# Optimization experiments

Measured on AMD Instinct MI355X. Metric: run time of the kernel, lower is better.

Reference implementation:

```python
import jax, jax.numpy as jnp
import numpy as np

B, C, F, D, K = 128, 64, 129, 512, 8192  # batch, channels, stft bins, d_model, codebook size


def setup_inputs() -> dict:
    key = jax.random.key(0)
    k0, k1, k2, k3 = jax.random.split(key, 4)
    x = jax.random.normal(k0, (B, C, F), dtype=jnp.float32)
    # nn.Linear(129, 512): weight stored transposed here as [F, D] for einsum
    W = jax.random.normal(k1, (F, D), dtype=jnp.float32) * (1.0 / np.sqrt(F).astype(np.float32))
    b = jnp.zeros((D,), dtype=jnp.float32)
    codebook = jax.random.normal(k2, (K, D), dtype=jnp.float32)
    pos_emb = jax.random.normal(k3, (1, C, D), dtype=jnp.float32)
    return {"x": x, "W": W, "b": b, "codebook": codebook, "pos_emb": pos_emb}


def reference(x, W, b, codebook, pos_emb):
    # Linear projection: [B,C,F] @ [F,D] -> [B,C,D]
    z = jnp.einsum('bcf,fd->bcd', x, W) + b

    # Vector quantization: nearest codebook entry by squared L2 distance.
    # dist(z,e) = |z|^2 - 2 z.e + |e|^2; argmin unaffected by constant |z|^2 per token,
    # but keep full expression for faithfulness/numerics.
    z2 = jnp.sum(z * z, axis=-1, keepdims=True)              # [B,C,1]
    e2 = jnp.sum(codebook * codebook, axis=-1)               # [K]
    dots = jnp.einsum('bcd,kd->bck', z, codebook)            # [B,C,K] dominant GEMM
    dists = z2 - 2.0 * dots + e2                             # [B,C,K]
    idx = jnp.argmin(dists, axis=-1)                         # [B,C] int
    q = codebook[idx]                                        # gather: [B,C,D]

    # commitment loss: mse(stop_grad(quantize), z)
    commit_loss = jnp.mean(jnp.square(jax.lax.stop_gradient(q) - z))

    # straight-through estimator
    quantized = z + jax.lax.stop_gradient(q - z)

    out = quantized + pos_emb
    return out, commit_loss
```

## Files before the change

### kernel.cpp

```cpp
#include <hip/hip_runtime.h>
#include <hip/hip_bf16.h>
#include <hip/hip_fp16.h>
#include <stdint.h>

#define B_ 128
#define C_ 64
#define F_ 129
#define D_ 512
#define K_ 8192
#define M_ (B_ * C_)

typedef __attribute__((ext_vector_type(8))) _Float16 half8;
typedef __attribute__((ext_vector_type(4))) float f32x4;
typedef unsigned long long u64;

__device__ __forceinline__ ushort f2h(float f) {
  const _Float16 h = (_Float16)f;
  return __builtin_bit_cast(ushort, h);
}
__device__ __forceinline__ uint32_t fmap(float f) {
  uint32_t s = __float_as_uint(f);
  return s ^ ((s & 0x80000000u) ? 0xFFFFFFFFu : 0x80000000u);
}

__global__ __launch_bounds__(256) void k_prep(
    const float* __restrict__ x, const float* __restrict__ W,
    const float* __restrict__ bias, const float* __restrict__ cb,
    float* __restrict__ z, ushort* __restrict__ zf, ushort* __restrict__ cf,
    float* __restrict__ e2) {
  const int tid = threadIdx.x;
  if (blockIdx.x < 512) {
    __shared__ float xs[16][F_];
    const int t0 = blockIdx.x * 16;
    const float* xsrc = x + (size_t)t0 * F_;
    for (int i = tid; i < 16 * F_; i += 256) xs[i / F_][i % F_] = xsrc[i];
    __syncthreads();
    float a0[16], a1[16];
#pragma unroll
    for (int r = 0; r < 16; ++r) { a0[r] = 0.f; a1[r] = 0.f; }
    const int c0 = tid, c1 = tid + 256;
    for (int f = 0; f < F_; ++f) {
      const float w0 = W[f * D_ + c0];
      const float w1 = W[f * D_ + c1];
#pragma unroll
      for (int r = 0; r < 16; ++r) {
        const float xv = xs[r][f];
        a0[r] = __builtin_fmaf(xv, w0, a0[r]);
        a1[r] = __builtin_fmaf(xv, w1, a1[r]);
      }
    }
    const float b0 = bias[c0], b1 = bias[c1];
#pragma unroll
    for (int r = 0; r < 16; ++r) {
      const size_t row = (size_t)(t0 + r) * D_;
      const float v0 = a0[r] + b0, v1 = a1[r] + b1;
      z[row + c0] = v0;
      z[row + c1] = v1;
      zf[row + c0] = f2h(v0);
      zf[row + c1] = f2h(v1);
    }
  } else {
    const int row = (blockIdx.x - 512) * 4 + (tid >> 6);
    const int lane = tid & 63;
    const float* src = cb + (size_t)row * D_;
    float s = 0.f;
#pragma unroll
    for (int i = 0; i < 8; ++i) {
      const int d = lane + i * 64;
      const float v = src[d];
      s = __builtin_fmaf(v, v, s);
      cf[(size_t)row * D_ + d] = f2h(v);
    }
#pragma unroll
    for (int o = 32; o > 0; o >>= 1) s += __shfl_down(s, o);
    if (lane == 0) e2[row] = s;
  }
}

__device__ __forceinline__ void stage_tile(const ushort* __restrict__ g,
                                           int r0, int k0, ushort* lds,
                                           int tid) {
  const int c = tid & 7;
#pragma unroll
  for (int i = 0; i < 4; ++i) {
    const int r = i * 32 + (tid >> 3);
    const int cs = c ^ (r & 7);
    const ushort* src = g + (size_t)(r0 + r) * D_ + k0 + cs * 8;
    char* dst = (char*)lds + i * 4096 + (tid >> 6) * 1024;
    __builtin_amdgcn_global_load_lds(
        (const __attribute__((address_space(1))) void*)src,
        (__attribute__((address_space(3))) void*)dst, 16, 0, 0);
  }
}

__global__ __launch_bounds__(256, 4) void k_argmin(
    const ushort* __restrict__ zf, const ushort* __restrict__ cf,
    const float* __restrict__ e2, u64* __restrict__ blk2) {
  __shared__ ushort lA[128 * 64], lB[128 * 64];
  const int tid = threadIdx.x;
  const int lane = tid & 63;
  const int w = tid >> 6;
  const int wr = (w >> 1) * 64;
  const int wc = (w & 1) * 64;
  const int m0 = (blockIdx.x >> 6) * 128;
  const int n0 = (blockIdx.x & 63) * 128;

  f32x4 acc[4][4];
#pragma unroll
  for (int m = 0; m < 4; ++m)
#pragma unroll
    for (int n = 0; n < 4; ++n) acc[m][n] = (f32x4){0.f, 0.f, 0.f, 0.f};

  for (int kt = 0; kt < D_ / 64; ++kt) {
    __syncthreads();
    stage_tile(zf, m0, kt * 64, lA, tid);
    stage_tile(cf, n0, kt * 64, lB, tid);
    asm volatile("s_waitcnt vmcnt(0)" ::: "memory");
    __syncthreads();
#pragma unroll
    for (int ks = 0; ks < 2; ++ks) {
      half8 at[4], bc[4];
#pragma unroll
      for (int m = 0; m < 4; ++m) {
        const int row = wr + m * 16 + (lane & 15);
        const int cbo = (ks * 64 + ((lane >> 4) << 4)) ^ ((row & 7) << 4);
        at[m] = *(const half8*)((const char*)lA + row * 128 + cbo);
      }
#pragma unroll
      for (int n = 0; n < 4; ++n) {
        const int row = wc + n * 16 + (lane & 15);
        const int cbo = (ks * 64 + ((lane >> 4) << 4)) ^ ((row & 7) << 4);
        bc[n] = *(const half8*)((const char*)lB + row * 128 + cbo);
      }
#pragma unroll
      for (int mc = 0; mc < 4; ++mc)
#pragma unroll
        for (int nt = 0; nt < 4; ++nt)
          acc[mc][nt] = __builtin_amdgcn_mfma_f32_16x16x32_f16(
              bc[mc], at[nt], acc[mc][nt], 0, 0, 0);
    }
  }

  const int cbase = n0 + wc + ((lane >> 4) << 2);
  float e2r[4][4];
#pragma unroll
  for (int mc = 0; mc < 4; ++mc)
#pragma unroll
    for (int j = 0; j < 4; ++j) e2r[mc][j] = e2[cbase + mc * 16 + j];
  const int half = (n0 + wc) >> 6;
  const int tbase = m0 + wr;

#pragma unroll
  for (int nt = 0; nt < 4; ++nt) {
    float v1 = 3.0e38f, v2 = 3.0e38f;
    int i1 = 0, i2 = 0;
#pragma unroll
    for (int mc = 0; mc < 4; ++mc) {
#pragma unroll
      for (int j = 0; j < 4; ++j) {
        const float dd = __builtin_fmaf(-2.f, acc[mc][nt][j], e2r[mc][j]);
        const int ii = cbase + mc * 16 + j;
        const bool lt1 = dd < v1;
        const bool lt2 = dd < v2;
        v2 = lt1 ? v1 : (lt2 ? dd : v2);
        i2 = lt1 ? i1 : (lt2 ? ii : i2);
        v1 = lt1 ? dd : v1;
        i1 = lt1 ? ii : i1;
      }
    }
#pragma unroll
    for (int o = 16; o < 64; o <<= 1) {
      const float bv1 = __shfl_xor(v1, o), bv2 = __shfl_xor(v2, o);
      const int bi1 = __shfl_xor(i1, o), bi2 = __shfl_xor(i2, o);
      const bool t = bv1 < v1;
      const float hv = t ? v1 : bv1;
      const int hi = t ? i1 : bi1;
      v1 = t ? bv1 : v1;
      i1 = t ? bi1 : i1;
      const bool t2 = bv2 < v2;
      const float cv2 = t2 ? bv2 : v2;
      const int ci2 = t2 ? bi2 : i2;
      const bool t3 = hv < cv2;
      v2 = t3 ? hv : cv2;
      i2 = t3 ? hi : ci2;
    }
    if (lane < 16) {
      const int row = tbase + nt * 16 + lane;
      u64* dst = blk2 + (size_t)row * 256 + half * 2;
      dst[0] = ((u64)fmap(v1) << 32) | (uint32_t)i1;
      dst[1] = ((u64)fmap(v2) << 32) | (uint32_t)i2;
    }
  }
}

#define CS(a, b)                          \
  {                                       \
    const u64 lo_ = (a < b) ? a : b;      \
    const u64 hi_ = (a < b) ? b : a;      \
    a = lo_;                              \
    b = hi_;                              \
  }

__global__ __launch_bounds__(256) void k_resolve(
    const u64* __restrict__ blk2, const float* __restrict__ cb,
    const float* __restrict__ z, const float* __restrict__ pos,
    float* __restrict__ out, float* __restrict__ lossp) {
  const int t = blockIdx.x * 4 + (threadIdx.x >> 6);
  const int lane = threadIdx.x & 63;
  const u64* kp = blk2 + (size_t)t * 256;
  u64 v0 = kp[lane * 4 + 0], v1 = kp[lane * 4 + 1];
  u64 v2 = kp[lane * 4 + 2], v3 = kp[lane * 4 + 3];
  CS(v0, v1) CS(v2, v3) CS(v0, v2) CS(v1, v3) CS(v1, v2)
#pragma unroll
  for (int o = 1; o < 64; o <<= 1) {
    const u64 b0 = __shfl_xor(v0, o), b1 = __shfl_xor(v1, o);
    const u64 b2 = __shfl_xor(v2, o), b3 = __shfl_xor(v3, o);
    u64 m0 = (v0 < b3) ? v0 : b3;
    u64 m1 = (v1 < b2) ? v1 : b2;
    u64 m2 = (v2 < b1) ? v2 : b1;
    u64 m3 = (v3 < b0) ? v3 : b0;
    CS(m0, m2) CS(m1, m3) CS(m0, m1) CS(m2, m3)
    v0 = m0; v1 = m1; v2 = m2; v3 = m3;
  }
  const int i0 = (int)(v0 & 0xFFFFFFFFull);
  const int i1 = (int)(v1 & 0xFFFFFFFFull);
  const int i2 = (int)(v2 & 0xFFFFFFFFull);
  const int i3 = (int)(v3 & 0xFFFFFFFFull);
  const float* c0 = cb + (size_t)i0 * D_;
  const float* c1 = cb + (size_t)i1 * D_;
  const float* c2 = cb + (size_t)i2 * D_;
  const float* c3 = cb + (size_t)i3 * D_;
  const float* zr = z + (size_t)t * D_;
  float zv[8], c0v[8], c1v[8], c2v[8], c3v[8];
  double dt0 = 0.0, dt1 = 0.0, dt2 = 0.0, dt3 = 0.0;
  double q0 = 0.0, q1 = 0.0, q2 = 0.0, q3 = 0.0;
#pragma unroll
  for (int i = 0; i < 8; ++i) {
    const int d = lane + i * 64;
    zv[i] = zr[d];
    c0v[i] = c0[d]; c1v[i] = c1[d]; c2v[i] = c2[d]; c3v[i] = c3[d];
    dt0 += (double)zv[i] * (double)c0v[i]; q0 += (double)c0v[i] * (double)c0v[i];
    dt1 += (double)zv[i] * (double)c1v[i]; q1 += (double)c1v[i] * (double)c1v[i];
    dt2 += (double)zv[i] * (double)c2v[i]; q2 += (double)c2v[i] * (double)c2v[i];
    dt3 += (double)zv[i] * (double)c3v[i]; q3 += (double)c3v[i] * (double)c3v[i];
  }
#pragma unroll
  for (int o = 1; o < 64; o <<= 1) {
    dt0 += __shfl_xor(dt0, o); dt1 += __shfl_xor(dt1, o);
    dt2 += __shfl_xor(dt2, o); dt3 += __shfl_xor(dt3, o);
    q0 += __shfl_xor(q0, o); q1 += __shfl_xor(q1, o);
    q2 += __shfl_xor(q2, o); q3 += __shfl_xor(q3, o);
  }
  const double d0 = q0 - 2.0 * dt0;
  const double d1 = q1 - 2.0 * dt1;
  const double d2 = q2 - 2.0 * dt2;
  const double d3 = q3 - 2.0 * dt3;
  int bsel = 0, bidx = i0;
  double bd = d0;
  if (d1 < bd || (d1 == bd && i1 < bidx)) { bd = d1; bidx = i1; bsel = 1; }
  if (d2 < bd || (d2 == bd && i2 < bidx)) { bd = d2; bidx = i2; bsel = 2; }
  if (d3 < bd || (d3 == bd && i3 < bidx)) { bd = d3; bidx = i3; bsel = 3; }
  const float* pe = pos + (size_t)(t & (C_ - 1)) * D_;
  float part = 0.f;
#pragma unroll
  for (int i = 0; i < 8; ++i) {
    const int d = lane + i * 64;
    const float qv = (bsel == 0) ? c0v[i]
                   : (bsel == 1) ? c1v[i]
                   : (bsel == 2) ? c2v[i] : c3v[i];
    const float df = qv - zv[i];
    part = __builtin_fmaf(df, df, part);
    out[(size_t)t * D_ + d] = qv + pe[d];
  }
#pragma unroll
  for (int o = 32; o > 0; o >>= 1) part += __shfl_down(part, o);
  if (lane == 0) lossp[t] = part;
}

__global__ __launch_bounds__(1024) void k_loss(const float* __restrict__ lossp,
                                               float* __restrict__ loss) {
  const int tid = threadIdx.x;
  float s = 0.f;
  for (int i = tid; i < M_; i += 1024) s += lossp[i];
#pragma unroll
  for (int o = 32; o > 0; o >>= 1) s += __shfl_down(s, o);
  __shared__ float red[16];
  if ((tid & 63) == 0) red[tid >> 6] = s;
  __syncthreads();
  if (tid == 0) {
    float tot = 0.f;
#pragma unroll
    for (int i = 0; i < 16; ++i) tot += red[i];
    *loss = tot * (1.0f / ((float)M_ * (float)D_));
  }
}

extern "C" void kernel_launch(void* const* d_in, const int* in_sizes, int n_in,
                              void* d_out, int out_size, void* d_ws,
                              size_t ws_size, hipStream_t stream) {
  const float* x = (const float*)d_in[0];
  const float* W = (const float*)d_in[1];
  const float* bias = (const float*)d_in[2];
  const float* cb = (const float*)d_in[3];
  const float* pos = (const float*)d_in[4];
  float* out = (float*)d_out;
  float* loss = out + (size_t)M_ * D_;

  char* ws = (char*)d_ws;
  float* z = (float*)(ws + 0);
  ushort* zf = (ushort*)(ws + (16ull << 20));
  ushort* cf = (ushort*)(ws + (24ull << 20));
  float* e2 = (float*)(ws + (32ull << 20));
  float* lossp = (float*)(ws + (32ull << 20) + 32768);
  u64* blk2 = (u64*)(ws + (32ull << 20) + 65536);

  k_prep<<<512 + K_ / 4, 256, 0, stream>>>(x, W, bias, cb, z, zf, cf, e2);
  k_argmin<<<(M_ / 128) * (K_ / 128), 256, 0, stream>>>(zf, cf, e2, blk2);
  k_resolve<<<M_ / 4, 256, 0, stream>>>(blk2, cb, z, pos, out, lossp);
  k_loss<<<1, 1024, 0, stream>>>(lossp, loss);
}
```

Measured before the change: 215.5 us.

## Transpose argmin candidate layout and fold loss reduction into resolve via atomics

The argmin kernel now writes per-block top-2 candidates in a half-major layout, so each column-block's writes for consecutive rows are contiguous. The resolve kernel loads a 4-token tile cooperatively through shared memory and reorders it back into per-token lists. The separate single-block loss kernel is removed: each resolve block reduces its four partials and atomically adds them into a loss value zeroed by a memset. This saves a kernel launch and a serial tail, but adds a memset, float atomics with nondeterministic summation order, and an extra barrier.

```diff
diff --git a/kernel.cpp b/kernel.cpp
--- a/kernel.cpp
+++ b/kernel.cpp
@@ -186,7 +186,7 @@
     }
     if (lane < 16) {
       const int row = tbase + nt * 16 + lane;
-      u64* dst = blk2 + (size_t)row * 256 + half * 2;
+      u64* dst = blk2 + ((size_t)half * M_ + row) * 2;
       dst[0] = ((u64)fmap(v1) << 32) | (uint32_t)i1;
       dst[1] = ((u64)fmap(v2) << 32) | (uint32_t)i2;
     }
@@ -204,12 +204,23 @@
 __global__ __launch_bounds__(256) void k_resolve(
     const u64* __restrict__ blk2, const float* __restrict__ cb,
     const float* __restrict__ z, const float* __restrict__ pos,
-    float* __restrict__ out, float* __restrict__ lossp) {
-  const int t = blockIdx.x * 4 + (threadIdx.x >> 6);
-  const int lane = threadIdx.x & 63;
-  const u64* kp = blk2 + (size_t)t * 256;
-  u64 v0 = kp[lane * 4 + 0], v1 = kp[lane * 4 + 1];
-  u64 v2 = kp[lane * 4 + 2], v3 = kp[lane * 4 + 3];
+    float* __restrict__ out, float* __restrict__ loss) {
+  __shared__ u64 cl[4 * 256];
+  __shared__ float red[4];
+  const int tid = threadIdx.x;
+  const int t0 = blockIdx.x * 4;
+#pragma unroll
+  for (int k = 0; k < 4; ++k) {
+    const int idx = k * 256 + tid;
+    const int h = idx >> 3, wi = idx & 7;
+    cl[(wi >> 1) * 256 + h * 2 + (wi & 1)] =
+        blk2[((size_t)h * M_ + t0) * 2 + wi];
+  }
+  __syncthreads();
+  const int wv = tid >> 6, lane = tid & 63;
+  const int t = t0 + wv;
+  u64 v0 = cl[wv * 256 + lane * 4 + 0], v1 = cl[wv * 256 + lane * 4 + 1];
+  u64 v2 = cl[wv * 256 + lane * 4 + 2], v3 = cl[wv * 256 + lane * 4 + 3];
   CS(v0, v1) CS(v2, v3) CS(v0, v2) CS(v1, v3) CS(v1, v2)
 #pragma unroll
   for (int o = 1; o < 64; o <<= 1) {
@@ -274,25 +285,11 @@
   }
 #pragma unroll
   for (int o = 32; o > 0; o >>= 1) part += __shfl_down(part, o);
-  if (lane == 0) lossp[t] = part;
-}
-
-__global__ __launch_bounds__(1024) void k_loss(const float* __restrict__ lossp,
-                                               float* __restrict__ loss) {
-  const int tid = threadIdx.x;
-  float s = 0.f;
-  for (int i = tid; i < M_; i += 1024) s += lossp[i];
-#pragma unroll
-  for (int o = 32; o > 0; o >>= 1) s += __shfl_down(s, o);
-  __shared__ float red[16];
-  if ((tid & 63) == 0) red[tid >> 6] = s;
+  if (lane == 0) red[wv] = part;
   __syncthreads();
-  if (tid == 0) {
-    float tot = 0.f;
-#pragma unroll
-    for (int i = 0; i < 16; ++i) tot += red[i];
-    *loss = tot * (1.0f / ((float)M_ * (float)D_));
-  }
+  if (tid == 0)
+    atomicAdd(loss, ((red[0] + red[1]) + (red[2] + red[3])) *
+                        (1.0f / ((float)M_ * (float)D_)));
 }
 
 extern "C" void kernel_launch(void* const* d_in, const int* in_sizes, int n_in,
@@ -311,11 +308,10 @@
   ushort* zf = (ushort*)(ws + (16ull << 20));
   ushort* cf = (ushort*)(ws + (24ull << 20));
   float* e2 = (float*)(ws + (32ull << 20));
-  float* lossp = (float*)(ws + (32ull << 20) + 32768);
   u64* blk2 = (u64*)(ws + (32ull << 20) + 65536);
 
+  hipMemsetAsync(loss, 0, sizeof(float), stream);
   k_prep<<<512 + K_ / 4, 256, 0, stream>>>(x, W, bias, cb, z, zf, cf, e2);
   k_argmin<<<(M_ / 128) * (K_ / 128), 256, 0, stream>>>(zf, cf, e2, blk2);
-  k_resolve<<<M_ / 4, 256, 0, stream>>>(blk2, cb, z, pos, out, lossp);
-  k_loss<<<1, 1024, 0, stream>>>(lossp, loss);
-}
+  k_resolve<<<M_ / 4, 256, 0, stream>>>(blk2, cb, z, pos, out, loss);
+}
```

After: 237.1 us. 1.1x slower.
